# Kernel tuning notes

Hardware: AMD Instinct MI355X
Metric: run time of the kernel (lower is better)

## Reference

```python
import jax, jax.numpy as jnp
import numpy as np

N_NODES = 100_000
N_EDGES = 1_600_000
N_GRAPHS = 1_000
VOCAB = 65
D_IN = 128
D_HID = 128


def setup_inputs() -> dict:
    key = jax.random.key(0)
    ks = jax.random.split(key, 12)
    x = jax.random.randint(ks[0], (N_NODES,), 0, VOCAB)
    edge_index = jax.random.randint(ks[1], (2, N_EDGES), 0, N_NODES)
    batch = jnp.sort(jax.random.randint(ks[2], (N_NODES,), 0, N_GRAPHS))

    def lin(k, fan_in, fan_out):
        bound = 1.0 / np.sqrt(fan_in)
        kw, kb = jax.random.split(k)
        W = jax.random.uniform(kw, (fan_in, fan_out), jnp.float32, -bound, bound)
        b = jax.random.uniform(kb, (fan_out,), jnp.float32, -bound, bound)
        return W, b

    emb = jax.random.normal(ks[3], (VOCAB, D_IN), jnp.float32)
    W1, b1 = lin(ks[4], D_IN, D_HID)
    W2, b2 = lin(ks[5], D_HID, D_HID)
    W3, b3 = lin(ks[6], D_HID, D_HID)
    Wf, bf = lin(ks[7], D_HID, 1)
    return {"x": x, "edge_index": edge_index, "batch": batch, "emb": emb,
            "W1": W1, "b1": b1, "W2": W2, "b2": b2, "W3": W3, "b3": b3,
            "Wf": Wf, "bf": bf}


def gcn_conv(h, W, b, src, dst, n):
    # PyG GCNConv: add self-loops, symmetric normalization D^-1/2 A_hat D^-1/2,
    # transform then aggregate messages at dst.
    h = h @ W                                             # [N, H]
    deg = jnp.zeros((n,), h.dtype).at[dst].add(1.0) + 1.0  # self-loop adds 1
    dinv = jax.lax.rsqrt(deg)                             # [N]
    coef = dinv[src] * dinv[dst]                          # [E]
    agg = jax.ops.segment_sum(h[src] * coef[:, None], dst, num_segments=n)
    return agg + h * (dinv * dinv)[:, None] + b           # self-loop term + bias


def reference(x, edge_index, batch, emb, W1, b1, W2, b2, W3, b3, Wf, bf):
    # Embedding with max_norm=1: renormalize looked-up rows to norm <= 1.
    e = emb[x]                                            # [N, D_IN]
    nrm = jnp.linalg.norm(e, axis=-1, keepdims=True)
    e = e * jnp.minimum(1.0, 1.0 / jnp.maximum(nrm, 1e-7))

    src, dst = edge_index[0], edge_index[1]
    h = jax.nn.relu(gcn_conv(e, W1, b1, src, dst, N_NODES))
    h = jax.nn.relu(gcn_conv(h, W2, b2, src, dst, N_NODES))
    h = jax.nn.relu(gcn_conv(h, W3, b3, src, dst, N_NODES))

    g = jax.ops.segment_max(h, batch, num_segments=N_GRAPHS)  # [G, H]
    return (g @ Wf + bf).ravel()                               # [G]
```

## Files before the change

kernel.cpp:

```cpp
#include <hip/hip_runtime.h>
#include <hip/hip_bf16.h>

#define N_NODES  100000
#define N_EDGES  1600000
#define N_GRAPHS 1000
#define D        128
#define CAP      64
#define NBKT     256
#define N_BUCKETS ((N_NODES + NBKT - 1) / NBKT)
#define HWGS     256
#define EPW      ((N_EDGES + HWGS - 1) / HWGS)
#define BNDB     ((N_NODES + 255) / 256)

typedef __attribute__((ext_vector_type(8))) short bf16x8;
typedef __attribute__((ext_vector_type(4))) float f32x4;

__device__ inline f32x4 mfma16(bf16x8 a, bf16x8 b, f32x4 c) {
    return __builtin_amdgcn_mfma_f32_16x16x32_bf16(a, b, c, 0, 0, 0);
}

__device__ inline unsigned short f2bf(float f) {
    unsigned u = __float_as_uint(f);
    unsigned r = u + 0x7fffu + ((u >> 16) & 1u);
    return (unsigned short)(r >> 16);
}

__global__ __launch_bounds__(256) void k_hist(const int* __restrict__ dst,
                                              int* __restrict__ bcnt,
                                              int* __restrict__ wgoff,
                                              const float* __restrict__ W1,
                                              const float* __restrict__ W2,
                                              const float* __restrict__ W3,
                                              short* __restrict__ frag,
                                              const int* __restrict__ batch,
                                              int* __restrict__ gstart,
                                              int* __restrict__ gend) {
    int w = blockIdx.x, t = threadIdx.x;
    if (w >= HWGS + 3) {
        int gid = (w - HWGS - 3) * 256 + t;
        if (gid < N_NODES) {
            int b = batch[gid];
            if (gid == 0 || batch[gid - 1] != b) gstart[b] = gid;
            if (gid == N_NODES - 1 || batch[gid + 1] != b) gend[b] = gid + 1;
        }
        return;
    }
    if (w >= HWGS) {
        int L = w - HWGS;
        const float* W = (L == 0) ? W1 : (L == 1) ? W2 : W3;
        short* fh = frag + (size_t)L * 32768;
        short* fl = fh + 16384;
        #pragma unroll
        for (int f = 0; f < 8; f++) {
            int id = t + f * 256;
            int lane = id & 63, kb = (id >> 6) & 3, nt = id >> 8;
            int k0 = kb * 32 + (lane >> 4) * 8;
            int n  = nt * 16 + (lane & 15);
            bf16x8 vh, vl;
            #pragma unroll
            for (int j = 0; j < 8; j++) {
                float wv = W[(k0 + j) * 128 + n];
                unsigned short hs = f2bf(wv);
                float hf = __uint_as_float((unsigned)hs << 16);
                vh[j] = (short)hs;
                vl[j] = (short)f2bf(wv - hf);
            }
            *(bf16x8*)&fh[id * 8] = vh;
            *(bf16x8*)&fl[id * 8] = vl;
        }
        return;
    }
    __shared__ int hist[N_BUCKETS];
    for (int b = t; b < N_BUCKETS; b += 256) hist[b] = 0;
    __syncthreads();
    int e0 = w * EPW, e1 = min(e0 + EPW, N_EDGES);
    for (int i = e0 + t; i < e1; i += 256)
        atomicAdd(&hist[dst[i] >> 8], 1);
    __syncthreads();
    for (int b = t; b < N_BUCKETS; b += 256) {
        int h = hist[b];
        wgoff[w * N_BUCKETS + b] = h ? atomicAdd(&bcnt[b], h) : 0;
    }
}

__global__ __launch_bounds__(512) void k_bscan(const int* __restrict__ bcnt,
                                               int* __restrict__ boff) {
    __shared__ int s[512];
    int t = threadIdx.x;
    int v = (t < N_BUCKETS) ? bcnt[t] : 0;
    s[t] = v;
    __syncthreads();
    for (int off = 1; off < 512; off <<= 1) {
        int val = (t >= off) ? s[t - off] : 0;
        __syncthreads();
        s[t] += val;
        __syncthreads();
    }
    if (t < N_BUCKETS) boff[t] = s[t] - v;
    if (t == 0) boff[N_BUCKETS] = N_EDGES;
}

__global__ __launch_bounds__(256) void k_scat(const int* __restrict__ src,
                                              const int* __restrict__ dst,
                                              const int* __restrict__ boff,
                                              const int* __restrict__ wgoff,
                                              int* __restrict__ ep) {
    __shared__ int cnt[N_BUCKETS];
    int t = threadIdx.x, w = blockIdx.x;
    for (int b = t; b < N_BUCKETS; b += 256) cnt[b] = 0;
    __syncthreads();
    int e0 = w * EPW, e1 = min(e0 + EPW, N_EDGES);
    for (int i = e0 + t; i < e1; i += 256) {
        int d = dst[i], b = d >> 8;
        int r = atomicAdd(&cnt[b], 1);
        ep[boff[b] + wgoff[w * N_BUCKETS + b] + r] = (src[i] << 8) | (d & 255);
    }
}

__global__ __launch_bounds__(256) void k_ell(const int* __restrict__ ep,
                                             const int* __restrict__ boff,
                                             int* __restrict__ ell,
                                             int* __restrict__ fill) {
    __shared__ int cnt_s[NBKT];
    __shared__ int ell_s[NBKT * CAP];
    int t = threadIdx.x, b = blockIdx.x;
    int nb0 = b * NBKT;
    int nn = min(NBKT, N_NODES - nb0);
    for (int i = t; i < NBKT; i += 256) cnt_s[i] = 0;
    __syncthreads();
    int e0 = boff[b], e1 = boff[b + 1];
    for (int i = e0 + t; i < e1; i += 256) {
        int e = ep[i];
        int ln = e & 255;
        int r = atomicAdd(&cnt_s[ln], 1);
        if (r < CAP) ell_s[ln * CAP + r] = (int)((unsigned)e >> 8);
    }
    __syncthreads();
    for (int i = t; i < nn * CAP; i += 256)
        ell[(size_t)nb0 * CAP + i] = ell_s[i];
    if (t < nn) fill[nb0 + t] = cnt_s[t];
}

__device__ inline void gemm_body(const short* Bh, const short* Bl,
                                 const bf16x8* a0, const bf16x8* a1,
                                 f32x4 acc[2][8], int lane) {
    #pragma unroll
    for (int kb = 0; kb < 4; kb++)
        #pragma unroll
        for (int nt = 0; nt < 8; nt++) {
            bf16x8 bh = *(const bf16x8*)&Bh[((nt * 4 + kb) * 64 + lane) * 8];
            bf16x8 bl = *(const bf16x8*)&Bl[((nt * 4 + kb) * 64 + lane) * 8];
            acc[0][nt] = mfma16(a0[kb], bh, acc[0][nt]);
            acc[0][nt] = mfma16(a0[kb], bl, acc[0][nt]);
            acc[1][nt] = mfma16(a1[kb], bh, acc[1][nt]);
            acc[1][nt] = mfma16(a1[kb], bl, acc[1][nt]);
        }
}

__device__ inline void gemm_epilogue(f32x4 acc[2][8], const int* fill,
                                     unsigned short* Cb, size_t r0,
                                     int quad, int col) {
    #pragma unroll
    for (int r = 0; r < 2; r++) {
        size_t row = r0 + r * 16 + quad * 4;
        #pragma unroll
        for (int g = 0; g < 4; g++) {
            float dv = (row + g < N_NODES)
                         ? 1.0f / sqrtf((float)fill[row + g] + 1.0f) : 0.f;
            #pragma unroll
            for (int nt = 0; nt < 8; nt++)
                Cb[(row + g) * D + nt * 16 + col] = f2bf(acc[r][nt][g] * dv);
        }
    }
}

__global__ __launch_bounds__(256) void k_gemm1e(const int* __restrict__ x,
                                                const float* __restrict__ emb,
                                                const short* __restrict__ frag,
                                                const int* __restrict__ fill,
                                                unsigned short* __restrict__ Cb) {
    __shared__ short Bfrag[2 * 16384];
    int t = threadIdx.x;
    {
        const int4* g4 = (const int4*)frag;
        int4* l4 = (int4*)Bfrag;
        #pragma unroll
        for (int i = 0; i < 16; i++) l4[t + i * 256] = g4[t + i * 256];
    }
    int w = t >> 6, lane = t & 63;
    int quad = lane >> 4, col = lane & 15;
    size_t r0 = (size_t)blockIdx.x * 128 + w * 32;

    bf16x8 a0[4], a1[4];
    {
        size_t ra = r0 + col, rb = r0 + 16 + col;
        int xa = (ra < N_NODES) ? x[ra] : 0;
        int xb = (rb < N_NODES) ? x[rb] : 0;
        float va[32], vb[32];
        float ssa = 0.f, ssb = 0.f;
        #pragma unroll
        for (int kb = 0; kb < 4; kb++) {
            float4 pa0 = *(const float4*)&emb[(size_t)xa * D + kb * 32 + quad * 8];
            float4 pa1 = *(const float4*)&emb[(size_t)xa * D + kb * 32 + quad * 8 + 4];
            float4 pb0 = *(const float4*)&emb[(size_t)xb * D + kb * 32 + quad * 8];
            float4 pb1 = *(const float4*)&emb[(size_t)xb * D + kb * 32 + quad * 8 + 4];
            va[kb*8+0]=pa0.x; va[kb*8+1]=pa0.y; va[kb*8+2]=pa0.z; va[kb*8+3]=pa0.w;
            va[kb*8+4]=pa1.x; va[kb*8+5]=pa1.y; va[kb*8+6]=pa1.z; va[kb*8+7]=pa1.w;
            vb[kb*8+0]=pb0.x; vb[kb*8+1]=pb0.y; vb[kb*8+2]=pb0.z; vb[kb*8+3]=pb0.w;
            vb[kb*8+4]=pb1.x; vb[kb*8+5]=pb1.y; vb[kb*8+6]=pb1.z; vb[kb*8+7]=pb1.w;
            #pragma unroll
            for (int j = 0; j < 8; j++) { ssa += va[kb*8+j]*va[kb*8+j];
                                          ssb += vb[kb*8+j]*vb[kb*8+j]; }
        }
        ssa += __shfl_xor(ssa, 16); ssa += __shfl_xor(ssa, 32);
        ssb += __shfl_xor(ssb, 16); ssb += __shfl_xor(ssb, 32);
        float sca = fminf(1.0f, 1.0f / fmaxf(sqrtf(ssa), 1e-7f));
        float scb = fminf(1.0f, 1.0f / fmaxf(sqrtf(ssb), 1e-7f));
        #pragma unroll
        for (int kb = 0; kb < 4; kb++) {
            bf16x8 fa, fb;
            #pragma unroll
            for (int j = 0; j < 8; j++) {
                fa[j] = (short)f2bf(va[kb*8+j] * sca);
                fb[j] = (short)f2bf(vb[kb*8+j] * scb);
            }
            a0[kb] = fa; a1[kb] = fb;
        }
    }
    f32x4 acc[2][8];
    #pragma unroll
    for (int r = 0; r < 2; r++)
        #pragma unroll
        for (int n = 0; n < 8; n++) acc[r][n] = (f32x4){0.f, 0.f, 0.f, 0.f};
    __syncthreads();
    gemm_body(Bfrag, Bfrag + 16384, a0, a1, acc, lane);
    gemm_epilogue(acc, fill, Cb, r0, quad, col);
}

__global__ __launch_bounds__(256) void k_gemm(const unsigned short* __restrict__ A,
                                              const short* __restrict__ frag,
                                              const int* __restrict__ fill,
                                              unsigned short* __restrict__ Cb) {
    __shared__ short Bfrag[2 * 16384];
    int t = threadIdx.x;
    {
        const int4* g4 = (const int4*)frag;
        int4* l4 = (int4*)Bfrag;
        #pragma unroll
        for (int i = 0; i < 16; i++) l4[t + i * 256] = g4[t + i * 256];
    }
    __syncthreads();
    int w = t >> 6, lane = t & 63;
    int quad = lane >> 4, col = lane & 15;
    size_t r0 = (size_t)blockIdx.x * 128 + w * 32;
    bf16x8 a0[4], a1[4];
    #pragma unroll
    for (int kb = 0; kb < 4; kb++) {
        a0[kb] = *(const bf16x8*)&A[(r0 + col)      * D + kb * 32 + quad * 8];
        a1[kb] = *(const bf16x8*)&A[(r0 + 16 + col) * D + kb * 32 + quad * 8];
    }
    f32x4 acc[2][8];
    #pragma unroll
    for (int r = 0; r < 2; r++)
        #pragma unroll
        for (int n = 0; n < 8; n++) acc[r][n] = (f32x4){0.f, 0.f, 0.f, 0.f};
    gemm_body(Bfrag, Bfrag + 16384, a0, a1, acc, lane);
    gemm_epilogue(acc, fill, Cb, r0, quad, col);
}

__device__ inline void acc8(float* acc, int4 r) {
    unsigned u0 = (unsigned)r.x, u1 = (unsigned)r.y,
             u2 = (unsigned)r.z, u3 = (unsigned)r.w;
    acc[0] += __uint_as_float(u0 << 16);
    acc[1] += __uint_as_float(u0 & 0xffff0000u);
    acc[2] += __uint_as_float(u1 << 16);
    acc[3] += __uint_as_float(u1 & 0xffff0000u);
    acc[4] += __uint_as_float(u2 << 16);
    acc[5] += __uint_as_float(u2 & 0xffff0000u);
    acc[6] += __uint_as_float(u3 << 16);
    acc[7] += __uint_as_float(u3 & 0xffff0000u);
}

#define LOADGRP(R, S, IT)                                                    \
    {                                                                        \
        _Pragma("unroll")                                                    \
        for (int k = 0; k < 4; k++) {                                        \
            int s = __shfl((S), (IT) * 16 + k * 4 + quad);                   \
            R[k] = *(const int4*)&hw2[((unsigned)s << 7) + cOff];            \
        }                                                                    \
    }
#define ACCGRP(A, R)                                                         \
    {                                                                        \
        _Pragma("unroll")                                                    \
        for (int k = 0; k < 4; k++) acc8((A), R[k]);                         \
    }

__global__ __launch_bounds__(256) void k_agg(const unsigned short* __restrict__ hw2,
                                             unsigned short* __restrict__ hout,
                                             const int* __restrict__ fill,
                                             const int* __restrict__ ell,
                                             const float* __restrict__ bias) {
    int w = threadIdx.x >> 6, lane = threadIdx.x & 63;
    int na = blockIdx.x * 8 + w * 2;
    int nb = na + 1;
    if (na >= N_NODES) return;
    int quad = lane >> 4;
    int l16  = lane & 15;
    unsigned cOff = (unsigned)(l16 << 3);

    int fa = __builtin_amdgcn_readfirstlane(fill[na]);
    int fb = __builtin_amdgcn_readfirstlane(fill[nb]);
    int ca = min(fa, CAP), cb = min(fb, CAP);
    int sa = (lane < ca) ? ell[na * CAP + lane] : N_NODES;
    int sb = (lane < cb) ? ell[nb * CAP + lane] : N_NODES;
    int ia = (ca + 15) >> 4; ia += (ia == 0);
    int ib = (cb + 15) >> 4; ib += (ib == 0);

    float accA[8], accB[8];
    #pragma unroll
    for (int c = 0; c < 8; c++) { accA[c] = 0.f; accB[c] = 0.f; }

    int4 A0[4], A1[4], B0[4], B1[4];
    LOADGRP(A0, sa, 0);
    LOADGRP(B0, sb, 0);
    if (1 < ia) LOADGRP(A1, sa, 1);
    ACCGRP(accA, A0);
    if (1 < ib) LOADGRP(B1, sb, 1);
    ACCGRP(accB, B0);
    if (ia > 1 || ib > 1) {
        if (2 < ia) LOADGRP(A0, sa, 2);
        if (1 < ia) ACCGRP(accA, A1);
        if (2 < ib) LOADGRP(B0, sb, 2);
        if (1 < ib) ACCGRP(accB, B1);
        if (ia > 2 || ib > 2) {
            if (3 < ia) LOADGRP(A1, sa, 3);
            if (2 < ia) ACCGRP(accA, A0);
            if (3 < ib) LOADGRP(B1, sb, 3);
            if (2 < ib) ACCGRP(accB, B0);
            if (3 < ia) ACCGRP(accA, A1);
            if (3 < ib) ACCGRP(accB, B1);
        }
    }

    #pragma unroll
    for (int c = 0; c < 8; c++) {
        accA[c] += __shfl_xor(accA[c], 16);
        accA[c] += __shfl_xor(accA[c], 32);
        accB[c] += __shfl_xor(accB[c], 16);
        accB[c] += __shfl_xor(accB[c], 32);
    }
    if (quad < 2) {
        int   n   = quad ? nb : na;
        int   fr  = quad ? fb : fa;
        float* acc = quad ? accB : accA;
        int4 sr = *(const int4*)&hw2[((unsigned)n << 7) + cOff];
        acc8(acc, sr);
        float di = 1.0f / sqrtf((float)fr + 1.0f);
        float4 bA = *(const float4*)&bias[l16 * 8];
        float4 bB = *(const float4*)&bias[l16 * 8 + 4];
        float o[8];
        o[0] = fmaxf(acc[0] * di + bA.x, 0.f);
        o[1] = fmaxf(acc[1] * di + bA.y, 0.f);
        o[2] = fmaxf(acc[2] * di + bA.z, 0.f);
        o[3] = fmaxf(acc[3] * di + bA.w, 0.f);
        o[4] = fmaxf(acc[4] * di + bB.x, 0.f);
        o[5] = fmaxf(acc[5] * di + bB.y, 0.f);
        o[6] = fmaxf(acc[6] * di + bB.z, 0.f);
        o[7] = fmaxf(acc[7] * di + bB.w, 0.f);
        int4 pk;
        pk.x = (int)((unsigned)f2bf(o[0]) | ((unsigned)f2bf(o[1]) << 16));
        pk.y = (int)((unsigned)f2bf(o[2]) | ((unsigned)f2bf(o[3]) << 16));
        pk.z = (int)((unsigned)f2bf(o[4]) | ((unsigned)f2bf(o[5]) << 16));
        pk.w = (int)((unsigned)f2bf(o[6]) | ((unsigned)f2bf(o[7]) << 16));
        *(int4*)&hout[((unsigned)n << 7) + cOff] = pk;
    }
}

__global__ __launch_bounds__(256) void k_pool(const unsigned short* __restrict__ h,
                                              const int* __restrict__ gstart,
                                              const int* __restrict__ gend,
                                              const float* __restrict__ Wf,
                                              const float* __restrict__ bf,
                                              float* __restrict__ out) {
    __shared__ float2 sm[4][64];
    int g = blockIdx.x;
    int w = threadIdx.x >> 6, lane = threadIdx.x & 63;
    int s = gstart[g], e = gend[g];
    float2 m = make_float2(-3.402823466e38f, -3.402823466e38f);
    for (int i = s + w; i < e; i += 4) {
        unsigned u = ((const unsigned*)(h + (size_t)i * D))[lane];
        m.x = fmaxf(m.x, __uint_as_float(u << 16));
        m.y = fmaxf(m.y, __uint_as_float(u & 0xffff0000u));
    }
    sm[w][lane] = m;
    __syncthreads();
    if (w == 0) {
        float2 a = sm[0][lane], b2 = sm[1][lane], c = sm[2][lane], d = sm[3][lane];
        m.x = fmaxf(fmaxf(a.x, b2.x), fmaxf(c.x, d.x));
        m.y = fmaxf(fmaxf(a.y, b2.y), fmaxf(c.y, d.y));
        float2 wf = ((const float2*)Wf)[lane];
        float val = m.x * wf.x + m.y * wf.y;
        #pragma unroll
        for (int off = 32; off; off >>= 1) val += __shfl_xor(val, off);
        if (lane == 0) out[g] = val + bf[0];
    }
}

extern "C" void kernel_launch(void* const* d_in, const int* in_sizes, int n_in,
                              void* d_out, int out_size, void* d_ws, size_t ws_size,
                              hipStream_t stream) {
    const int*   x    = (const int*)d_in[0];
    const int*   ei   = (const int*)d_in[1];
    const int*   batch= (const int*)d_in[2];
    const float* emb  = (const float*)d_in[3];
    const float* W1   = (const float*)d_in[4];
    const float* b1   = (const float*)d_in[5];
    const float* W2   = (const float*)d_in[6];
    const float* b2   = (const float*)d_in[7];
    const float* W3   = (const float*)d_in[8];
    const float* b3   = (const float*)d_in[9];
    const float* Wf   = (const float*)d_in[10];
    const float* bf   = (const float*)d_in[11];
    float* out = (float*)d_out;

    const int* src = ei;
    const int* dst = ei + N_EDGES;

    char* p = (char*)d_ws;
    unsigned short* hAb  = (unsigned short*)p; p += (size_t)(N_NODES + 128) * D * 2;
    unsigned short* hwb  = (unsigned short*)p; p += (size_t)(N_NODES + 128) * D * 2;
    int*            ep   = (int*)hwb;
    int*   fill     = (int*)p;              p += (size_t)N_NODES * 4;
    int*   gbounds  = (int*)p;              p += (size_t)2 * N_GRAPHS * 4;
    int*   ell      = (int*)p;              p += (size_t)N_NODES * CAP * 4;
    int*   wgoff    = (int*)p;              p += (size_t)HWGS * N_BUCKETS * 4;
    int*   bcnt     = (int*)p;              p += (size_t)(N_BUCKETS + 4) * 4;
    int*   boff     = (int*)p;              p += (size_t)(N_BUCKETS + 4) * 4;
    short* wfrag    = (short*)p;            p += (size_t)3 * 32768 * 2;
    (void)p;
    int* gstart = gbounds;
    int* gend   = gbounds + N_GRAPHS;

    hipMemsetAsync(bcnt, 0, (size_t)N_BUCKETS * 4, stream);
    hipMemsetAsync(gbounds, 0x7f, (size_t)2 * N_GRAPHS * 4, stream);

    const int GB = (N_NODES + 127) / 128;
    const int AB = N_NODES / 8;

    k_hist <<<HWGS + 3 + BNDB, 256, 0, stream>>>(dst, bcnt, wgoff, W1, W2, W3,
                                                 wfrag, batch, gstart, gend);
    k_bscan<<<1, 512, 0, stream>>>(bcnt, boff);
    k_scat <<<HWGS, 256, 0, stream>>>(src, dst, boff, wgoff, ep);
    k_ell  <<<N_BUCKETS, 256, 0, stream>>>(ep, boff, ell, fill);

    k_gemm1e<<<GB, 256, 0, stream>>>(x, emb, wfrag, fill, hwb);
    k_agg   <<<AB, 256, 0, stream>>>(hwb, hAb, fill, ell, b1);
    k_gemm<<<GB, 256, 0, stream>>>(hAb, wfrag + 32768, fill, hwb);
    k_agg <<<AB, 256, 0, stream>>>(hwb, hAb, fill, ell, b2);
    k_gemm<<<GB, 256, 0, stream>>>(hAb, wfrag + 65536, fill, hwb);
    k_agg <<<AB, 256, 0, stream>>>(hwb, hAb, fill, ell, b3);

    k_pool<<<N_GRAPHS, 256, 0, stream>>>(hAb, gstart, gend, Wf, bf, out);
}
```

Measured before the change: 375.8 us.

## Drop split-bf16 weights, fold bucket scan into scatter/ELL kernels, skip bounds memset

Weights are now packed as a single bf16 fragment instead of a hi/lo pair. This halves the MFMA count and the LDS staging in the three GEMM kernels, at the cost of lower weight precision. The separate bucket-scan kernel is removed: k_scat recomputes the prefix scan in shared memory, and k_ell reduces the preceding bucket counts itself. The memset that initialised the graph bounds is also dropped, which assumes every graph owns at least one node.

Result: no change. 374.5 us, median of 2 (-0.4%).

```diff
diff --git a/kernel.cpp b/kernel.cpp
--- a/kernel.cpp
+++ b/kernel.cpp
@@ -48,25 +48,18 @@
     if (w >= HWGS) {
         int L = w - HWGS;
         const float* W = (L == 0) ? W1 : (L == 1) ? W2 : W3;
-        short* fh = frag + (size_t)L * 32768;
-        short* fl = fh + 16384;
+        short* fh = frag + (size_t)L * 16384;
         #pragma unroll
         for (int f = 0; f < 8; f++) {
             int id = t + f * 256;
             int lane = id & 63, kb = (id >> 6) & 3, nt = id >> 8;
             int k0 = kb * 32 + (lane >> 4) * 8;
             int n  = nt * 16 + (lane & 15);
-            bf16x8 vh, vl;
+            bf16x8 vh;
             #pragma unroll
-            for (int j = 0; j < 8; j++) {
-                float wv = W[(k0 + j) * 128 + n];
-                unsigned short hs = f2bf(wv);
-                float hf = __uint_as_float((unsigned)hs << 16);
-                vh[j] = (short)hs;
-                vl[j] = (short)f2bf(wv - hf);
-            }
+            for (int j = 0; j < 8; j++)
+                vh[j] = (short)f2bf(W[(k0 + j) * 128 + n]);
             *(bf16x8*)&fh[id * 8] = vh;
-            *(bf16x8*)&fl[id * 8] = vl;
         }
         return;
     }
@@ -83,52 +76,59 @@
     }
 }
 
-__global__ __launch_bounds__(512) void k_bscan(const int* __restrict__ bcnt,
-                                               int* __restrict__ boff) {
-    __shared__ int s[512];
-    int t = threadIdx.x;
-    int v = (t < N_BUCKETS) ? bcnt[t] : 0;
-    s[t] = v;
-    __syncthreads();
-    for (int off = 1; off < 512; off <<= 1) {
-        int val = (t >= off) ? s[t - off] : 0;
-        __syncthreads();
-        s[t] += val;
-        __syncthreads();
-    }
-    if (t < N_BUCKETS) boff[t] = s[t] - v;
-    if (t == 0) boff[N_BUCKETS] = N_EDGES;
-}
-
 __global__ __launch_bounds__(256) void k_scat(const int* __restrict__ src,
                                               const int* __restrict__ dst,
-                                              const int* __restrict__ boff,
+                                              const int* __restrict__ bcnt,
                                               const int* __restrict__ wgoff,
                                               int* __restrict__ ep) {
+    __shared__ int sc[2][512];
+    __shared__ int boff_s[N_BUCKETS];
     __shared__ int cnt[N_BUCKETS];
     int t = threadIdx.x, w = blockIdx.x;
+    for (int i = t; i < 512; i += 256) sc[0][i] = (i < N_BUCKETS) ? bcnt[i] : 0;
     for (int b = t; b < N_BUCKETS; b += 256) cnt[b] = 0;
+    __syncthreads();
+    int pp = 0;
+    for (int off = 1; off < 512; off <<= 1) {
+        for (int i = t; i < 512; i += 256) {
+            int v = sc[pp][i];
+            if (i >= off) v += sc[pp][i - off];
+            sc[1 - pp][i] = v;
+        }
+        __syncthreads();
+        pp ^= 1;
+    }
+    for (int i = t; i < N_BUCKETS; i += 256) boff_s[i] = i ? sc[pp][i - 1] : 0;
     __syncthreads();
     int e0 = w * EPW, e1 = min(e0 + EPW, N_EDGES);
     for (int i = e0 + t; i < e1; i += 256) {
         int d = dst[i], b = d >> 8;
         int r = atomicAdd(&cnt[b], 1);
-        ep[boff[b] + wgoff[w * N_BUCKETS + b] + r] = (src[i] << 8) | (d & 255);
+        ep[boff_s[b] + wgoff[w * N_BUCKETS + b] + r] = (src[i] << 8) | (d & 255);
     }
 }
 
 __global__ __launch_bounds__(256) void k_ell(const int* __restrict__ ep,
-                                             const int* __restrict__ boff,
+                                             const int* __restrict__ bcnt,
                                              int* __restrict__ ell,
                                              int* __restrict__ fill) {
+    __shared__ int red[256];
     __shared__ int cnt_s[NBKT];
     __shared__ int ell_s[NBKT * CAP];
     int t = threadIdx.x, b = blockIdx.x;
+    int partial = 0;
+    for (int i = t; i < b; i += 256) partial += bcnt[i];
+    red[t] = partial;
+    for (int i = t; i < NBKT; i += 256) cnt_s[i] = 0;
+    __syncthreads();
+    for (int off = 128; off; off >>= 1) {
+        if (t < off) red[t] += red[t + off];
+        __syncthreads();
+    }
+    int e0 = red[0];
+    int e1 = e0 + bcnt[b];
     int nb0 = b * NBKT;
     int nn = min(NBKT, N_NODES - nb0);
-    for (int i = t; i < NBKT; i += 256) cnt_s[i] = 0;
-    __syncthreads();
-    int e0 = boff[b], e1 = boff[b + 1];
     for (int i = e0 + t; i < e1; i += 256) {
         int e = ep[i];
         int ln = e & 255;
@@ -141,19 +141,16 @@
     if (t < nn) fill[nb0 + t] = cnt_s[t];
 }
 
-__device__ inline void gemm_body(const short* Bh, const short* Bl,
+__device__ inline void gemm_body(const short* Bf,
                                  const bf16x8* a0, const bf16x8* a1,
                                  f32x4 acc[2][8], int lane) {
     #pragma unroll
     for (int kb = 0; kb < 4; kb++)
         #pragma unroll
         for (int nt = 0; nt < 8; nt++) {
-            bf16x8 bh = *(const bf16x8*)&Bh[((nt * 4 + kb) * 64 + lane) * 8];
-            bf16x8 bl = *(const bf16x8*)&Bl[((nt * 4 + kb) * 64 + lane) * 8];
-            acc[0][nt] = mfma16(a0[kb], bh, acc[0][nt]);
-            acc[0][nt] = mfma16(a0[kb], bl, acc[0][nt]);
-            acc[1][nt] = mfma16(a1[kb], bh, acc[1][nt]);
-            acc[1][nt] = mfma16(a1[kb], bl, acc[1][nt]);
+            bf16x8 b = *(const bf16x8*)&Bf[((nt * 4 + kb) * 64 + lane) * 8];
+            acc[0][nt] = mfma16(a0[kb], b, acc[0][nt]);
+            acc[1][nt] = mfma16(a1[kb], b, acc[1][nt]);
         }
 }
 
@@ -179,13 +176,13 @@
                                                 const short* __restrict__ frag,
                                                 const int* __restrict__ fill,
                                                 unsigned short* __restrict__ Cb) {
-    __shared__ short Bfrag[2 * 16384];
+    __shared__ short Bfrag[16384];
     int t = threadIdx.x;
     {
         const int4* g4 = (const int4*)frag;
         int4* l4 = (int4*)Bfrag;
         #pragma unroll
-        for (int i = 0; i < 16; i++) l4[t + i * 256] = g4[t + i * 256];
+        for (int i = 0; i < 8; i++) l4[t + i * 256] = g4[t + i * 256];
     }
     int w = t >> 6, lane = t & 63;
     int quad = lane >> 4, col = lane & 15;
@@ -233,7 +230,7 @@
         #pragma unroll
         for (int n = 0; n < 8; n++) acc[r][n] = (f32x4){0.f, 0.f, 0.f, 0.f};
     __syncthreads();
-    gemm_body(Bfrag, Bfrag + 16384, a0, a1, acc, lane);
+    gemm_body(Bfrag, a0, a1, acc, lane);
     gemm_epilogue(acc, fill, Cb, r0, quad, col);
 }
 
@@ -241,13 +238,13 @@
                                               const short* __restrict__ frag,
                                               const int* __restrict__ fill,
                                               unsigned short* __restrict__ Cb) {
-    __shared__ short Bfrag[2 * 16384];
+    __shared__ short Bfrag[16384];
     int t = threadIdx.x;
     {
         const int4* g4 = (const int4*)frag;
         int4* l4 = (int4*)Bfrag;
         #pragma unroll
-        for (int i = 0; i < 16; i++) l4[t + i * 256] = g4[t + i * 256];
+        for (int i = 0; i < 8; i++) l4[t + i * 256] = g4[t + i * 256];
     }
     __syncthreads();
     int w = t >> 6, lane = t & 63;
@@ -264,7 +261,7 @@
     for (int r = 0; r < 2; r++)
         #pragma unroll
         for (int n = 0; n < 8; n++) acc[r][n] = (f32x4){0.f, 0.f, 0.f, 0.f};
-    gemm_body(Bfrag, Bfrag + 16384, a0, a1, acc, lane);
+    gemm_body(Bfrag, a0, a1, acc, lane);
     gemm_epilogue(acc, fill, Cb, r0, quad, col);
 }
 
@@ -435,29 +432,26 @@
     int*   ell      = (int*)p;              p += (size_t)N_NODES * CAP * 4;
     int*   wgoff    = (int*)p;              p += (size_t)HWGS * N_BUCKETS * 4;
     int*   bcnt     = (int*)p;              p += (size_t)(N_BUCKETS + 4) * 4;
-    int*   boff     = (int*)p;              p += (size_t)(N_BUCKETS + 4) * 4;
-    short* wfrag    = (short*)p;            p += (size_t)3 * 32768 * 2;
+    short* wfrag    = (short*)p;            p += (size_t)3 * 16384 * 2;
     (void)p;
     int* gstart = gbounds;
     int* gend   = gbounds + N_GRAPHS;
 
     hipMemsetAsync(bcnt, 0, (size_t)N_BUCKETS * 4, stream);
-    hipMemsetAsync(gbounds, 0x7f, (size_t)2 * N_GRAPHS * 4, stream);
 
     const int GB = (N_NODES + 127) / 128;
     const int AB = N_NODES / 8;
 
-    k_hist <<<HWGS + 3 + BNDB, 256, 0, stream>>>(dst, bcnt, wgoff, W1, W2, W3,
-                                                 wfrag, batch, gstart, gend);
-    k_bscan<<<1, 512, 0, stream>>>(bcnt, boff);
-    k_scat <<<HWGS, 256, 0, stream>>>(src, dst, boff, wgoff, ep);
-    k_ell  <<<N_BUCKETS, 256, 0, stream>>>(ep, boff, ell, fill);
+    k_hist<<<HWGS + 3 + BNDB, 256, 0, stream>>>(dst, bcnt, wgoff, W1, W2, W3,
+                                                wfrag, batch, gstart, gend);
+    k_scat<<<HWGS, 256, 0, stream>>>(src, dst, bcnt, wgoff, ep);
+    k_ell <<<N_BUCKETS, 256, 0, stream>>>(ep, bcnt, ell, fill);
 
     k_gemm1e<<<GB, 256, 0, stream>>>(x, emb, wfrag, fill, hwb);
     k_agg   <<<AB, 256, 0, stream>>>(hwb, hAb, fill, ell, b1);
+    k_gemm<<<GB, 256, 0, stream>>>(hAb, wfrag + 16384, fill, hwb);
+    k_agg <<<AB, 256, 0, stream>>>(hwb, hAb, fill, ell, b2);
     k_gemm<<<GB, 256, 0, stream>>>(hAb, wfrag + 32768, fill, hwb);
-    k_agg <<<AB, 256, 0, stream>>>(hwb, hAb, fill, ell, b2);
-    k_gemm<<<GB, 256, 0, stream>>>(hAb, wfrag + 65536, fill, hwb);
     k_agg <<<AB, 256, 0, stream>>>(hwb, hAb, fill, ell, b3);
 
     k_pool<<<N_GRAPHS, 256, 0, stream>>>(hAb, gstart, gend, Wf, bf, out);
```
